# Optimization experiments

Measured on AMD Instinct MI355X. Metric: run time of the kernel, lower is better.

The kernel has to match this reference:

```python
import jax, jax.numpy as jnp
import numpy as np

D = 1024      # d_model
H = 2         # num_heads
DH = D // H   # head dim


def setup_inputs() -> dict:
    key = jax.random.key(0)
    ks = jax.random.split(key, 16)
    B, N = 512, 512
    s = 0.02
    return {
        "h": jax.random.normal(ks[0], (B, D), jnp.float32),
        "c": jax.random.normal(ks[1], (B, D), jnp.float32),
        "all_states": jax.random.normal(ks[2], (B, N, D), jnp.float32),
        "external_input": jax.random.normal(ks[3], (B, D), jnp.float32),
        # nn.MultiheadAttention params
        "in_proj_w": jax.random.normal(ks[4], (3 * D, D), jnp.float32) * s,
        "in_proj_b": jnp.zeros((3 * D,), jnp.float32),
        "out_proj_w": jax.random.normal(ks[5], (D, D), jnp.float32) * s,
        "out_proj_b": jnp.zeros((D,), jnp.float32),
        # nn.LSTMCell params (gate order: i, f, g, o)
        "w_ih": jax.random.normal(ks[6], (4 * D, 2 * D), jnp.float32) * s,
        "b_ih": jnp.zeros((4 * D,), jnp.float32),
        "w_hh": jax.random.normal(ks[7], (4 * D, D), jnp.float32) * s,
        "b_hh": jnp.zeros((4 * D,), jnp.float32),
        # ln_out params
        "ln_w": jnp.ones((D,), jnp.float32),
        "ln_b": jnp.zeros((D,), jnp.float32),
    }


def _layer_norm(x, w, b, eps=1e-5):
    mu = jnp.mean(x, axis=-1, keepdims=True)
    var = jnp.var(x, axis=-1, keepdims=True)
    return (x - mu) * jax.lax.rsqrt(var + eps) * w + b


def reference(h, c, all_states, external_input,
              in_proj_w, in_proj_b, out_proj_w, out_proj_b,
              w_ih, b_ih, w_hh, b_hh, ln_w, ln_b):
    B, N, _ = all_states.shape
    wq, wk, wv = in_proj_w[:D], in_proj_w[D:2 * D], in_proj_w[2 * D:]
    bq, bk, bv = in_proj_b[:D], in_proj_b[D:2 * D], in_proj_b[2 * D:]

    # single-query multi-head attention over all_states
    q = (h @ wq.T + bq).reshape(B, H, DH)                     # [B,H,Dh]
    k = (all_states @ wk.T + bk).reshape(B, N, H, DH)          # [B,N,H,Dh]
    v = (all_states @ wv.T + bv).reshape(B, N, H, DH)
    scores = jnp.einsum("bhd,bnhd->bhn", q, k) / jnp.sqrt(jnp.float32(DH))
    attn = jax.nn.softmax(scores, axis=-1)                     # [B,H,N]
    ctx = jnp.einsum("bhn,bnhd->bhd", attn, v).reshape(B, D)
    context = ctx @ out_proj_w.T + out_proj_b                  # [B,D]

    # LSTMCell on cat([context, external_input])
    rnn_in = jnp.concatenate([context, external_input], axis=-1)  # [B,2D]
    gates = rnn_in @ w_ih.T + b_ih + h @ w_hh.T + b_hh            # [B,4D]
    i, f, g, o = jnp.split(gates, 4, axis=-1)
    new_c = jax.nn.sigmoid(f) * c + jax.nn.sigmoid(i) * jnp.tanh(g)
    new_h = jax.nn.sigmoid(o) * jnp.tanh(new_c)

    return _layer_norm(new_h, ln_w, ln_b), new_c
```

## Files before the change

### kernel.cpp

```cpp
#include <hip/hip_runtime.h>
#include <math.h>
#include <stdint.h>

constexpr int kD  = 1024;
constexpr int kB  = 512;
constexpr int kN  = 512;
constexpr int kDH = 512;

using bf16x8 = __attribute__((ext_vector_type(8))) short;
using f32x4v = __attribute__((ext_vector_type(4))) float;
using us8    = __attribute__((ext_vector_type(8))) unsigned short;
using us4    = __attribute__((ext_vector_type(4))) unsigned short;

__device__ __forceinline__ unsigned short f2bf(float f) {
    uint32_t u = __float_as_uint(f);
    u += 0x7fffu + ((u >> 16) & 1u);
    return (unsigned short)(u >> 16);
}

__device__ __forceinline__ float bf2f(unsigned short s) {
    return __uint_as_float((uint32_t)s << 16);
}

__device__ __forceinline__ void async16(const void* g, void* l) {
    __builtin_amdgcn_global_load_lds(
        (const __attribute__((address_space(1))) uint32_t*)g,
        (__attribute__((address_space(3))) uint32_t*)l, 16, 0, 0);
}

__global__ __launch_bounds__(256)
void cvt_bf16(const float* __restrict__ src, unsigned short* __restrict__ dst,
              int scols8, int dcols, int coloff, int n8)
{
    int idx = blockIdx.x * 256 + threadIdx.x;
    if (idx >= n8) return;
    int row = idx / scols8;
    int c = (idx - row * scols8) * 8;
    const float4* s = (const float4*)(src + (long)row * ((long)scols8 * 8) + c);
    float4 v0 = s[0], v1 = s[1];
    us8 o;
    o[0] = f2bf(v0.x); o[1] = f2bf(v0.y); o[2] = f2bf(v0.z); o[3] = f2bf(v0.w);
    o[4] = f2bf(v1.x); o[5] = f2bf(v1.y); o[6] = f2bf(v1.z); o[7] = f2bf(v1.w);
    *(us8*)(dst + (long)row * dcols + coloff + c) = o;
}

__global__ __launch_bounds__(256)
void tcvt_wk(const float* __restrict__ wk, unsigned short* __restrict__ dst)
{
    __shared__ float t[32][33];
    const int nt = blockIdx.x;
    const int kt = blockIdx.y;
    const int hh = blockIdx.z;
    const int tx = threadIdx.x & 31, ty = threadIdx.x >> 5;
    const float scale = 0.044194173824159216f;
#pragma unroll
    for (int j = 0; j < 4; ++j)
        t[ty + j * 8][tx] = wk[(long)(hh * 512 + kt * 32 + ty + j * 8) * kD + nt * 32 + tx];
    __syncthreads();
#pragma unroll
    for (int j = 0; j < 4; ++j) {
        int n = nt * 32 + ty + j * 8;
        int k = kt * 32 + tx;
        dst[(long)hh * 524288 + (long)n * 512 + k] = f2bf(t[tx][ty + j * 8] * scale);
    }
}

__global__ __launch_bounds__(256)
void gemm64(const unsigned short* __restrict__ A, int lda, long sAz,
            const unsigned short* __restrict__ B, int ldb, long sBz,
            float* __restrict__ Cf, int ldcf, long sCfz,
            unsigned short* __restrict__ Cb, int ldcb, long sCbz,
            const float* __restrict__ bias, long sbz, int K)
{
    __shared__ short As[4][64][8];
    __shared__ short Bs[4][64][8];
    A += (long)blockIdx.z * sAz;
    B += (long)blockIdx.z * sBz;

    const int tid = threadIdx.x;
    const int l = tid & 63, w = tid >> 6;
    const int wr = w >> 1, wc = w & 1;
    const int bm = blockIdx.y * 64, bn = blockIdx.x * 64;

    f32x4v acc[2][2] = {};

    for (int k0 = 0; k0 < K; k0 += 32) {
        __syncthreads();
        {
            int ks = tid >> 6, r = tid & 63;
            async16(A + (long)(bm + r) * lda + k0 + ks * 8, (short*)As + (long)tid * 8);
            async16(B + (long)(bn + r) * ldb + k0 + ks * 8, (short*)Bs + (long)tid * 8);
        }
        __syncthreads();

        const int ks = l >> 4, rr = l & 15;
        bf16x8 a[2], b[2];
#pragma unroll
        for (int t = 0; t < 2; ++t) {
            a[t] = *(const bf16x8*)&As[ks][wr * 32 + t * 16 + rr][0];
            b[t] = *(const bf16x8*)&Bs[ks][wc * 32 + t * 16 + rr][0];
        }
#pragma unroll
        for (int mt = 0; mt < 2; ++mt)
#pragma unroll
            for (int nt = 0; nt < 2; ++nt)
                acc[mt][nt] = __builtin_amdgcn_mfma_f32_16x16x32_bf16(
                    a[mt], b[nt], acc[mt][nt], 0, 0, 0);
    }

    const int rr = l & 15, rg = l >> 4;
#pragma unroll
    for (int mt = 0; mt < 2; ++mt) {
#pragma unroll
        for (int nt = 0; nt < 2; ++nt) {
            const int n = bn + wc * 32 + nt * 16 + rr;
            float bb = bias ? bias[(long)blockIdx.z * sbz + n] : 0.f;
#pragma unroll
            for (int r = 0; r < 4; ++r) {
                const int m = bm + wr * 32 + mt * 16 + rg * 4 + r;
                float val = acc[mt][nt][r] + bb;
                if (Cf) Cf[(long)blockIdx.z * sCfz + (long)m * ldcf + n] = val;
                if (Cb) Cb[(long)blockIdx.z * sCbz + (long)m * ldcb + n] = f2bf(val);
            }
        }
    }
}

__global__ __launch_bounds__(256)
void gemm_gates64(const unsigned short* __restrict__ A, int lda,
                  const unsigned short* __restrict__ B, int ldb,
                  float* __restrict__ Cf, int ldcf,
                  const float* __restrict__ b1, const float* __restrict__ b2,
                  int K)
{
    __shared__ short As[8][64][8];
    __shared__ short Bs[8][64][8];

    const int tid = threadIdx.x;
    const int l = tid & 63, w = tid >> 6;
    const int wr = w >> 1, wc = w & 1;
    const int bm = blockIdx.y * 64, bn = blockIdx.x * 64;

    f32x4v acc[2][2] = {};

    for (int k0 = 0; k0 < K; k0 += 64) {
        __syncthreads();
#pragma unroll
        for (int j = 0; j < 2; ++j) {
            int ca = j * 256 + tid;
            int ks = ca >> 6, r = ca & 63;
            async16(A + (long)(bm + r) * lda + k0 + ks * 8, (short*)As + (long)ca * 8);
            async16(B + (long)(bn + r) * ldb + k0 + ks * 8, (short*)Bs + (long)ca * 8);
        }
        __syncthreads();

        const int ksl = l >> 4, rr = l & 15;
#pragma unroll
        for (int p = 0; p < 2; ++p) {
            bf16x8 a[2], b[2];
#pragma unroll
            for (int t = 0; t < 2; ++t) {
                a[t] = *(const bf16x8*)&As[p * 4 + ksl][wr * 32 + t * 16 + rr][0];
                b[t] = *(const bf16x8*)&Bs[p * 4 + ksl][wc * 32 + t * 16 + rr][0];
            }
#pragma unroll
            for (int mt = 0; mt < 2; ++mt)
#pragma unroll
                for (int nt = 0; nt < 2; ++nt)
                    acc[mt][nt] = __builtin_amdgcn_mfma_f32_16x16x32_bf16(
                        a[mt], b[nt], acc[mt][nt], 0, 0, 0);
        }
    }

    const int rr = l & 15, rg = l >> 4;
#pragma unroll
    for (int mt = 0; mt < 2; ++mt) {
#pragma unroll
        for (int nt = 0; nt < 2; ++nt) {
            const int n = bn + wc * 32 + nt * 16 + rr;
            const float bb = b1[n] + b2[n];
#pragma unroll
            for (int r = 0; r < 4; ++r) {
                const int m = bm + wr * 32 + mt * 16 + rg * 4 + r;
                Cf[(long)m * ldcf + n] = acc[mt][nt][r] + bb;
            }
        }
    }
}

__global__ __launch_bounds__(512, 4)
void attn7(const float* __restrict__ xall,
           const float* __restrict__ qt,
           unsigned short* __restrict__ spart_bf,
           float* __restrict__ mlpart)
{
    const int b = blockIdx.x;
    const int tid = threadIdx.x;
    const int w = tid >> 6, l = tid & 63;

    float qa[16], qb[16];
    {
        const float* qp = qt + (long)b * 2048 + l * 4;
#pragma unroll
        for (int q = 0; q < 4; ++q) {
            float4 v0 = *(const float4*)(qp + q * 256);
            float4 v1 = *(const float4*)(qp + 1024 + q * 256);
            qa[q*4+0] = v0.x; qa[q*4+1] = v0.y; qa[q*4+2] = v0.z; qa[q*4+3] = v0.w;
            qb[q*4+0] = v1.x; qb[q*4+1] = v1.y; qb[q*4+2] = v1.z; qb[q*4+3] = v1.w;
        }
    }

    float m0 = -1e30f, l0 = 0.f, m1 = -1e30f, l1 = 0.f;
    float sa[16] = {}, sb[16] = {};

    const float* xr = xall + ((long)b * kN + w * 64) * kD + l * 4;

    for (int r = 0; r < 64; ++r) {
        float xv[16];
#pragma unroll
        for (int q = 0; q < 4; ++q) {
            float4 v = *(const float4*)(xr + q * 256);
            xv[q*4+0] = v.x; xv[q*4+1] = v.y; xv[q*4+2] = v.z; xv[q*4+3] = v.w;
        }
        xr += kD;

        float c0=0.f,c1=0.f,c2=0.f,c3=0.f, e0=0.f,e1=0.f,e2=0.f,e3=0.f;
#pragma unroll
        for (int q = 0; q < 4; ++q) {
            c0 += xv[q*4+0]*qa[q*4+0]; c1 += xv[q*4+1]*qa[q*4+1];
            c2 += xv[q*4+2]*qa[q*4+2]; c3 += xv[q*4+3]*qa[q*4+3];
            e0 += xv[q*4+0]*qb[q*4+0]; e1 += xv[q*4+1]*qb[q*4+1];
            e2 += xv[q*4+2]*qb[q*4+2]; e3 += xv[q*4+3]*qb[q*4+3];
        }
        float d0 = (c0 + c1) + (c2 + c3);
        float d1 = (e0 + e1) + (e2 + e3);
#pragma unroll
        for (int mm = 32; mm >= 1; mm >>= 1) {
            d0 += __shfl_xor(d0, mm);
            d1 += __shfl_xor(d1, mm);
        }

        if (d0 > m0 + 8.f) {
            float rsc = __expf(m0 - d0);
            l0 *= rsc;
#pragma unroll
            for (int j = 0; j < 16; ++j) sa[j] *= rsc;
            m0 = d0;
        }
        float p0 = __expf(d0 - m0);
        l0 += p0;

        if (d1 > m1 + 8.f) {
            float rsc = __expf(m1 - d1);
            l1 *= rsc;
#pragma unroll
            for (int j = 0; j < 16; ++j) sb[j] *= rsc;
            m1 = d1;
        }
        float p1 = __expf(d1 - m1);
        l1 += p1;

#pragma unroll
        for (int j = 0; j < 16; ++j) {
            sa[j] += p0 * xv[j];
            sb[j] += p1 * xv[j];
        }
    }

    unsigned short* sp0 = spart_bf + (((long)b * 8 + w) * 2 + 0) * 1024 + l * 4;
    unsigned short* sp1 = spart_bf + (((long)b * 8 + w) * 2 + 1) * 1024 + l * 4;
#pragma unroll
    for (int q = 0; q < 4; ++q) {
        us4 o0, o1;
        o0[0] = f2bf(sa[q*4+0]); o0[1] = f2bf(sa[q*4+1]);
        o0[2] = f2bf(sa[q*4+2]); o0[3] = f2bf(sa[q*4+3]);
        o1[0] = f2bf(sb[q*4+0]); o1[1] = f2bf(sb[q*4+1]);
        o1[2] = f2bf(sb[q*4+2]); o1[3] = f2bf(sb[q*4+3]);
        *(us4*)(sp0 + q * 256) = o0;
        *(us4*)(sp1 + q * 256) = o1;
    }

    if (l == 0) {
        float* mlp = mlpart + (((long)b * 8 + w) * 2) * 2;
        mlp[0] = m0; mlp[1] = l0; mlp[2] = m1; mlp[3] = l1;
    }
}

__global__ __launch_bounds__(256)
void attn_combine8(const unsigned short* __restrict__ spart_bf,
                   const float* __restrict__ mlpart,
                   unsigned short* __restrict__ sac_bf)
{
    const int b = blockIdx.x;
    const int tid = threadIdx.x;
    const int h = tid >> 7, d0 = (tid & 127) * 8;

    float m[8], lv[8];
#pragma unroll
    for (int c = 0; c < 8; ++c) {
        const float* mlp = mlpart + (((long)b * 8 + c) * 2 + h) * 2;
        m[c] = mlp[0]; lv[c] = mlp[1];
    }
    float ms = m[0];
#pragma unroll
    for (int c = 1; c < 8; ++c) ms = fmaxf(ms, m[c]);
    float wgt[8], L = 0.f;
#pragma unroll
    for (int c = 0; c < 8; ++c) { wgt[c] = __expf(m[c] - ms); L += wgt[c] * lv[c]; }
    const float inv = 1.0f / L;

    float acc[8] = {};
#pragma unroll
    for (int c = 0; c < 8; ++c) {
        us8 sv = *(const us8*)(spart_bf + (((long)b * 8 + c) * 2 + h) * 1024 + d0);
#pragma unroll
        for (int j = 0; j < 8; ++j)
            acc[j] += wgt[c] * bf2f(sv[j]);
    }
    us8 o;
#pragma unroll
    for (int j = 0; j < 8; ++j) o[j] = f2bf(acc[j] * inv);
    *(us8*)(sac_bf + (long)b * 2048 + h * kD + d0) = o;
}

__device__ __forceinline__ float sigm(float x) { return 1.0f / (1.0f + __expf(-x)); }

__global__ __launch_bounds__(256)
void lstm_ln(const float* __restrict__ gates, const float* __restrict__ cin,
             const float* __restrict__ ln_w, const float* __restrict__ ln_b,
             float* __restrict__ out0, float* __restrict__ out1)
{
    __shared__ float red[2][4];
    __shared__ float stats[2];

    const int b = blockIdx.x;
    const int tid = threadIdx.x;
    const int d4 = tid * 4;
    const float* g = gates + (long)b * 4096;

    float4 gi = *(const float4*)(g + d4);
    float4 gf = *(const float4*)(g + 1024 + d4);
    float4 gg = *(const float4*)(g + 2048 + d4);
    float4 go = *(const float4*)(g + 3072 + d4);
    float4 cv = *(const float4*)(cin + (long)b * kD + d4);

    float iv[4] = {gi.x, gi.y, gi.z, gi.w};
    float fv[4] = {gf.x, gf.y, gf.z, gf.w};
    float gv[4] = {gg.x, gg.y, gg.z, gg.w};
    float ov[4] = {go.x, go.y, go.z, go.w};
    float cc[4] = {cv.x, cv.y, cv.z, cv.w};

    float nc[4], nh[4];
#pragma unroll
    for (int u = 0; u < 4; ++u) {
        nc[u] = sigm(fv[u]) * cc[u] + sigm(iv[u]) * tanhf(gv[u]);
        nh[u] = sigm(ov[u]) * tanhf(nc[u]);
    }
    *(float4*)(out1 + (long)b * kD + d4) = make_float4(nc[0], nc[1], nc[2], nc[3]);

    float sum = nh[0] + nh[1] + nh[2] + nh[3];
    float ss  = nh[0]*nh[0] + nh[1]*nh[1] + nh[2]*nh[2] + nh[3]*nh[3];
#pragma unroll
    for (int m = 32; m >= 1; m >>= 1) {
        sum += __shfl_xor(sum, m);
        ss  += __shfl_xor(ss, m);
    }
    const int wave = tid >> 6, lane = tid & 63;
    if (lane == 0) { red[0][wave] = sum; red[1][wave] = ss; }
    __syncthreads();
    if (tid == 0) {
        float s = red[0][0] + red[0][1] + red[0][2] + red[0][3];
        float q = red[1][0] + red[1][1] + red[1][2] + red[1][3];
        float mu = s / (float)kD;
        float var = q / (float)kD - mu * mu;
        stats[0] = mu;
        stats[1] = rsqrtf(var + 1e-5f);
    }
    __syncthreads();
    const float mu = stats[0], rstd = stats[1];
    float4 lw = *(const float4*)(ln_w + d4);
    float4 lb = *(const float4*)(ln_b + d4);
    float lwv[4] = {lw.x, lw.y, lw.z, lw.w};
    float lbv[4] = {lb.x, lb.y, lb.z, lb.w};
    float o[4];
#pragma unroll
    for (int u = 0; u < 4; ++u)
        o[u] = (nh[u] - mu) * rstd * lwv[u] + lbv[u];
    *(float4*)(out0 + (long)b * kD + d4) = make_float4(o[0], o[1], o[2], o[3]);
}

extern "C" void kernel_launch(void* const* d_in, const int* in_sizes, int n_in,
                              void* d_out, int out_size, void* d_ws, size_t ws_size,
                              hipStream_t stream)
{
    (void)in_sizes; (void)n_in; (void)out_size;

    const float* h    = (const float*)d_in[0];
    const float* c    = (const float*)d_in[1];
    const float* xall = (const float*)d_in[2];
    const float* ext  = (const float*)d_in[3];
    const float* in_w = (const float*)d_in[4];
    const float* in_b = (const float*)d_in[5];
    const float* wo   = (const float*)d_in[6];
    const float* bo   = (const float*)d_in[7];
    const float* w_ih = (const float*)d_in[8];
    const float* b_ih = (const float*)d_in[9];
    const float* w_hh = (const float*)d_in[10];
    const float* b_hh = (const float*)d_in[11];
    const float* ln_w = (const float*)d_in[12];
    const float* ln_b = (const float*)d_in[13];

    float* out0 = (float*)d_out;
    float* out1 = out0 + (long)kB * kD;

    char* p = (char*)d_ws;
    const size_t need = 63062016ull;
    if (ws_size < need) return;

    p += 16384;
    unsigned short* h_bf   = (unsigned short*)p; p += 1048576;
    unsigned short* wq_bf  = (unsigned short*)p; p += 2097152;
    unsigned short* wkT_bf = (unsigned short*)p; p += 2097152;
    unsigned short* wv_bf  = (unsigned short*)p; p += 2097152;
    unsigned short* wo_bf  = (unsigned short*)p; p += 2097152;
    unsigned short* q_bf   = (unsigned short*)p; p += 1048576;
    unsigned short* sac_bf = (unsigned short*)p; p += 2097152;
    unsigned short* ctx_bf = (unsigned short*)p; p += 1048576;
    unsigned short* acat   = (unsigned short*)p; p += 3145728;
    unsigned short* wcat   = (unsigned short*)p; p += 25165824;
    char* ov = p;
    float*          qtl      = (float*)ov;
    unsigned short* spart_bf = (unsigned short*)(ov + 4194304);
    float*          mlpart   = (float*)(ov + 4194304 + 16777216);
    float*          gates    = (float*)ov;

    const float* wk_f = in_w + (long)kD * kD;
    const float* bq = in_b;
    const float* bv = in_b + 2 * kD;

    auto cvt = [&](const float* src, unsigned short* dst, int rows, int scols,
                   int dcols, int coloff) {
        int n8 = rows * (scols / 8);
        cvt_bf16<<<(n8 + 255) / 256, 256, 0, stream>>>(src, dst, scols / 8, dcols, coloff, n8);
    };

    cvt(h, h_bf, 512, 1024, 1024, 0);
    cvt(in_w, wq_bf, 1024, 1024, 1024, 0);
    tcvt_wk<<<dim3(32, 16, 2), 256, 0, stream>>>(wk_f, wkT_bf);
    cvt(in_w + 2L * kD * kD, wv_bf, 1024, 1024, 1024, 0);
    cvt(wo, wo_bf, 1024, 1024, 1024, 0);
    cvt(w_ih, wcat, 4096, 2048, 3072, 0);
    cvt(w_hh, wcat, 4096, 1024, 3072, 2048);

    gemm64<<<dim3(16, 8, 1), 256, 0, stream>>>(
        h_bf, 1024, 0, wq_bf, 1024, 0,
        nullptr, 0, 0, q_bf, 1024, 0, bq, 0, 1024);

    gemm64<<<dim3(16, 8, 2), 256, 0, stream>>>(
        q_bf, 1024, 512, wkT_bf, 512, 524288,
        qtl, 2048, 1024, nullptr, 0, 0, nullptr, 0, 512);

    attn7<<<kB, 512, 0, stream>>>(xall, qtl, spart_bf, mlpart);

    attn_combine8<<<kB, 256, 0, stream>>>(spart_bf, mlpart, sac_bf);

    gemm64<<<dim3(8, 8, 2), 256, 0, stream>>>(
        sac_bf, 2048, 1024, wv_bf, 1024, 524288,
        nullptr, 0, 0, ctx_bf, 1024, 512, bv, 512, 1024);

    gemm64<<<dim3(16, 8, 1), 256, 0, stream>>>(
        ctx_bf, 1024, 0, wo_bf, 1024, 0,
        nullptr, 0, 0, acat, 3072, 0, bo, 0, 1024);

    cvt(ext, acat, 512, 1024, 3072, 1024);
    cvt(h,   acat, 512, 1024, 3072, 2048);

    gemm_gates64<<<dim3(64, 8), 256, 0, stream>>>(
        acat, 3072, wcat, 3072, gates, 4096, b_ih, b_hh, 3072);

    lstm_ln<<<kB, 256, 0, stream>>>(gates, c, ln_w, ln_b, out0, out1);
}
```

Before: 396.5 us.

## Halve GEMM M-tiles and split-K the gates GEMM to fill more CUs

The small projection GEMMs now use 32x64 tiles instead of 64x64, doubling the number of blocks launched. The LSTM gates GEMM is split along K into two halves that write separate partial outputs. The LSTM/LayerNorm kernel now sums the two partials and adds both biases. The aim is better occupancy on the many-CU GPU for these small GEMMs, at the cost of less reuse per tile and an extra read and write of the gates buffers.

```diff
diff --git a/kernel.cpp b/kernel.cpp
--- a/kernel.cpp
+++ b/kernel.cpp
@@ -66,91 +66,83 @@
 }
 
 __global__ __launch_bounds__(256)
-void gemm64(const unsigned short* __restrict__ A, int lda, long sAz,
+void gemm32(const unsigned short* __restrict__ A, int lda, long sAz,
             const unsigned short* __restrict__ B, int ldb, long sBz,
             float* __restrict__ Cf, int ldcf, long sCfz,
             unsigned short* __restrict__ Cb, int ldcb, long sCbz,
             const float* __restrict__ bias, long sbz, int K)
 {
-    __shared__ short As[4][64][8];
+    __shared__ short As[4][32][8];
     __shared__ short Bs[4][64][8];
     A += (long)blockIdx.z * sAz;
     B += (long)blockIdx.z * sBz;
+
+    const int tid = threadIdx.x;
+    const int l = tid & 63, w = tid >> 6;
+    const int wr = w >> 1, wc = w & 1;
+    const int bm = blockIdx.y * 32, bn = blockIdx.x * 64;
+
+    f32x4v acc[2] = {};
+
+    for (int k0 = 0; k0 < K; k0 += 32) {
+        __syncthreads();
+        if (tid < 128) {
+            int ks = tid >> 5, r = tid & 31;
+            async16(A + (long)(bm + r) * lda + k0 + ks * 8, (short*)As + (long)tid * 8);
+        }
+        {
+            int ks = tid >> 6, r = tid & 63;
+            async16(B + (long)(bn + r) * ldb + k0 + ks * 8, (short*)Bs + (long)tid * 8);
+        }
+        __syncthreads();
+
+        const int ks = l >> 4, rr = l & 15;
+        bf16x8 a  = *(const bf16x8*)&As[ks][wr * 16 + rr][0];
+        bf16x8 b0 = *(const bf16x8*)&Bs[ks][wc * 32 + rr][0];
+        bf16x8 b1 = *(const bf16x8*)&Bs[ks][wc * 32 + 16 + rr][0];
+        acc[0] = __builtin_amdgcn_mfma_f32_16x16x32_bf16(a, b0, acc[0], 0, 0, 0);
+        acc[1] = __builtin_amdgcn_mfma_f32_16x16x32_bf16(a, b1, acc[1], 0, 0, 0);
+    }
+
+    const int rr = l & 15, rg = l >> 4;
+#pragma unroll
+    for (int nt = 0; nt < 2; ++nt) {
+        const int n = bn + wc * 32 + nt * 16 + rr;
+        float bb = bias ? bias[(long)blockIdx.z * sbz + n] : 0.f;
+#pragma unroll
+        for (int r = 0; r < 4; ++r) {
+            const int m = bm + wr * 16 + rg * 4 + r;
+            float val = acc[nt][r] + bb;
+            if (Cf) Cf[(long)blockIdx.z * sCfz + (long)m * ldcf + n] = val;
+            if (Cb) Cb[(long)blockIdx.z * sCbz + (long)m * ldcb + n] = f2bf(val);
+        }
+    }
+}
+
+__global__ __launch_bounds__(256)
+void gemm_gates_sk(const unsigned short* __restrict__ A, int lda,
+                   const unsigned short* __restrict__ B, int ldb,
+                   float* __restrict__ Cf, int ldcf, long sCfz)
+{
+    __shared__ short As[8][64][8];
+    __shared__ short Bs[8][64][8];
 
     const int tid = threadIdx.x;
     const int l = tid & 63, w = tid >> 6;
     const int wr = w >> 1, wc = w & 1;
     const int bm = blockIdx.y * 64, bn = blockIdx.x * 64;
+    const int kbase = blockIdx.z * 1536;
 
     f32x4v acc[2][2] = {};
 
-    for (int k0 = 0; k0 < K; k0 += 32) {
-        __syncthreads();
-        {
-            int ks = tid >> 6, r = tid & 63;
-            async16(A + (long)(bm + r) * lda + k0 + ks * 8, (short*)As + (long)tid * 8);
-            async16(B + (long)(bn + r) * ldb + k0 + ks * 8, (short*)Bs + (long)tid * 8);
-        }
-        __syncthreads();
-
-        const int ks = l >> 4, rr = l & 15;
-        bf16x8 a[2], b[2];
-#pragma unroll
-        for (int t = 0; t < 2; ++t) {
-            a[t] = *(const bf16x8*)&As[ks][wr * 32 + t * 16 + rr][0];
-            b[t] = *(const bf16x8*)&Bs[ks][wc * 32 + t * 16 + rr][0];
-        }
-#pragma unroll
-        for (int mt = 0; mt < 2; ++mt)
-#pragma unroll
-            for (int nt = 0; nt < 2; ++nt)
-                acc[mt][nt] = __builtin_amdgcn_mfma_f32_16x16x32_bf16(
-                    a[mt], b[nt], acc[mt][nt], 0, 0, 0);
-    }
-
-    const int rr = l & 15, rg = l >> 4;
-#pragma unroll
-    for (int mt = 0; mt < 2; ++mt) {
-#pragma unroll
-        for (int nt = 0; nt < 2; ++nt) {
-            const int n = bn + wc * 32 + nt * 16 + rr;
-            float bb = bias ? bias[(long)blockIdx.z * sbz + n] : 0.f;
-#pragma unroll
-            for (int r = 0; r < 4; ++r) {
-                const int m = bm + wr * 32 + mt * 16 + rg * 4 + r;
-                float val = acc[mt][nt][r] + bb;
-                if (Cf) Cf[(long)blockIdx.z * sCfz + (long)m * ldcf + n] = val;
-                if (Cb) Cb[(long)blockIdx.z * sCbz + (long)m * ldcb + n] = f2bf(val);
-            }
-        }
-    }
-}
-
-__global__ __launch_bounds__(256)
-void gemm_gates64(const unsigned short* __restrict__ A, int lda,
-                  const unsigned short* __restrict__ B, int ldb,
-                  float* __restrict__ Cf, int ldcf,
-                  const float* __restrict__ b1, const float* __restrict__ b2,
-                  int K)
-{
-    __shared__ short As[8][64][8];
-    __shared__ short Bs[8][64][8];
-
-    const int tid = threadIdx.x;
-    const int l = tid & 63, w = tid >> 6;
-    const int wr = w >> 1, wc = w & 1;
-    const int bm = blockIdx.y * 64, bn = blockIdx.x * 64;
-
-    f32x4v acc[2][2] = {};
-
-    for (int k0 = 0; k0 < K; k0 += 64) {
+    for (int k0 = 0; k0 < 1536; k0 += 64) {
         __syncthreads();
 #pragma unroll
         for (int j = 0; j < 2; ++j) {
             int ca = j * 256 + tid;
             int ks = ca >> 6, r = ca & 63;
-            async16(A + (long)(bm + r) * lda + k0 + ks * 8, (short*)As + (long)ca * 8);
-            async16(B + (long)(bn + r) * ldb + k0 + ks * 8, (short*)Bs + (long)ca * 8);
+            async16(A + (long)(bm + r) * lda + kbase + k0 + ks * 8, (short*)As + (long)ca * 8);
+            async16(B + (long)(bn + r) * ldb + kbase + k0 + ks * 8, (short*)Bs + (long)ca * 8);
         }
         __syncthreads();
 
@@ -173,16 +165,16 @@
     }
 
     const int rr = l & 15, rg = l >> 4;
+    float* Cz = Cf + (long)blockIdx.z * sCfz;
 #pragma unroll
     for (int mt = 0; mt < 2; ++mt) {
 #pragma unroll
         for (int nt = 0; nt < 2; ++nt) {
             const int n = bn + wc * 32 + nt * 16 + rr;
-            const float bb = b1[n] + b2[n];
 #pragma unroll
             for (int r = 0; r < 4; ++r) {
                 const int m = bm + wr * 32 + mt * 16 + rg * 4 + r;
-                Cf[(long)m * ldcf + n] = acc[mt][nt][r] + bb;
+                Cz[(long)m * ldcf + n] = acc[mt][nt][r];
             }
         }
     }
@@ -326,9 +318,11 @@
 __device__ __forceinline__ float sigm(float x) { return 1.0f / (1.0f + __expf(-x)); }
 
 __global__ __launch_bounds__(256)
-void lstm_ln(const float* __restrict__ gates, const float* __restrict__ cin,
-             const float* __restrict__ ln_w, const float* __restrict__ ln_b,
-             float* __restrict__ out0, float* __restrict__ out1)
+void lstm_ln2(const float* __restrict__ gA, const float* __restrict__ gB,
+              const float* __restrict__ b_ih, const float* __restrict__ b_hh,
+              const float* __restrict__ cin,
+              const float* __restrict__ ln_w, const float* __restrict__ ln_b,
+              float* __restrict__ out0, float* __restrict__ out1)
 {
     __shared__ float red[2][4];
     __shared__ float stats[2];
@@ -336,18 +330,24 @@
     const int b = blockIdx.x;
     const int tid = threadIdx.x;
     const int d4 = tid * 4;
-    const float* g = gates + (long)b * 4096;
-
-    float4 gi = *(const float4*)(g + d4);
-    float4 gf = *(const float4*)(g + 1024 + d4);
-    float4 gg = *(const float4*)(g + 2048 + d4);
-    float4 go = *(const float4*)(g + 3072 + d4);
+    const float* ga = gA + (long)b * 4096;
+    const float* gb = gB + (long)b * 4096;
+
+    float iv[4], fv[4], gv[4], ov[4];
+#pragma unroll
+    for (int gidx = 0; gidx < 4; ++gidx) {
+        const int off = gidx * 1024 + d4;
+        float4 a = *(const float4*)(ga + off);
+        float4 bq = *(const float4*)(gb + off);
+        float4 bi = *(const float4*)(b_ih + off);
+        float4 bh = *(const float4*)(b_hh + off);
+        float* dstv = (gidx == 0) ? iv : (gidx == 1) ? fv : (gidx == 2) ? gv : ov;
+        dstv[0] = a.x + bq.x + bi.x + bh.x;
+        dstv[1] = a.y + bq.y + bi.y + bh.y;
+        dstv[2] = a.z + bq.z + bi.z + bh.z;
+        dstv[3] = a.w + bq.w + bi.w + bh.w;
+    }
     float4 cv = *(const float4*)(cin + (long)b * kD + d4);
-
-    float iv[4] = {gi.x, gi.y, gi.z, gi.w};
-    float fv[4] = {gf.x, gf.y, gf.z, gf.w};
-    float gv[4] = {gg.x, gg.y, gg.z, gg.w};
-    float ov[4] = {go.x, go.y, go.z, go.w};
     float cc[4] = {cv.x, cv.y, cv.z, cv.w};
 
     float nc[4], nh[4];
@@ -432,7 +432,8 @@
     float*          qtl      = (float*)ov;
     unsigned short* spart_bf = (unsigned short*)(ov + 4194304);
     float*          mlpart   = (float*)(ov + 4194304 + 16777216);
-    float*          gates    = (float*)ov;
+    float*          gatesA   = (float*)ov;
+    float*          gatesB   = (float*)(ov + 8388608);
 
     const float* wk_f = in_w + (long)kD * kD;
     const float* bq = in_b;
@@ -452,11 +453,11 @@
     cvt(w_ih, wcat, 4096, 2048, 3072, 0);
     cvt(w_hh, wcat, 4096, 1024, 3072, 2048);
 
-    gemm64<<<dim3(16, 8, 1), 256, 0, stream>>>(
+    gemm32<<<dim3(16, 16, 1), 256, 0, stream>>>(
         h_bf, 1024, 0, wq_bf, 1024, 0,
         nullptr, 0, 0, q_bf, 1024, 0, bq, 0, 1024);
 
-    gemm64<<<dim3(16, 8, 2), 256, 0, stream>>>(
+    gemm32<<<dim3(16, 16, 2), 256, 0, stream>>>(
         q_bf, 1024, 512, wkT_bf, 512, 524288,
         qtl, 2048, 1024, nullptr, 0, 0, nullptr, 0, 512);
 
@@ -464,19 +465,20 @@
 
     attn_combine8<<<kB, 256, 0, stream>>>(spart_bf, mlpart, sac_bf);
 
-    gemm64<<<dim3(8, 8, 2), 256, 0, stream>>>(
+    gemm32<<<dim3(8, 16, 2), 256, 0, stream>>>(
         sac_bf, 2048, 1024, wv_bf, 1024, 524288,
         nullptr, 0, 0, ctx_bf, 1024, 512, bv, 512, 1024);
 
-    gemm64<<<dim3(16, 8, 1), 256, 0, stream>>>(
+    gemm32<<<dim3(16, 16, 1), 256, 0, stream>>>(
         ctx_bf, 1024, 0, wo_bf, 1024, 0,
         nullptr, 0, 0, acat, 3072, 0, bo, 0, 1024);
 
     cvt(ext, acat, 512, 1024, 3072, 1024);
     cvt(h,   acat, 512, 1024, 3072, 2048);
 
-    gemm_gates64<<<dim3(64, 8), 256, 0, stream>>>(
-        acat, 3072, wcat, 3072, gates, 4096, b_ih, b_hh, 3072);
-
-    lstm_ln<<<kB, 256, 0, stream>>>(gates, c, ln_w, ln_b, out0, out1);
-}
+    gemm_gates_sk<<<dim3(64, 8, 2), 256, 0, stream>>>(
+        acat, 3072, wcat, 3072, gatesA, 4096, 2097152);
+
+    lstm_ln2<<<kB, 256, 0, stream>>>(gatesA, gatesB, b_ih, b_hh,
+                                     c, ln_w, ln_b, out0, out1);
+}
```

Result: no change. 390.4 us (-1.6%).
